# Performance work log

Hardware: AMD Instinct MI355X
Metric: run time of the kernel (lower is better)

The kernel has to match this reference:

```python
import jax, jax.numpy as jnp
import numpy as np

N_NODES = 50000
N_EDGES = 800000
DIM = 128
N_GRAPHS = 512
LEVELS = [2, 2, 2]  # GCN layers per hierarchy level
N_LAYERS = sum(LEVELS)
EPS = 1e-5


def setup_inputs() -> dict:
    key = jax.random.key(0)
    ks = jax.random.split(key, 8)
    x = jax.random.normal(ks[0], (N_NODES, DIM), dtype=jnp.float32)
    edge_index = jax.random.randint(ks[1], (2, N_EDGES), 0, N_NODES, dtype=jnp.int64)
    batch = jnp.sort(jax.random.randint(ks[2], (N_NODES,), 0, N_GRAPHS, dtype=jnp.int64))
    # stacked per-layer GCN params (all layers are DIM->DIM since input_dim==hidden_dim)
    s = 1.0 / np.sqrt(DIM)
    W = jax.random.uniform(ks[3], (N_LAYERS, DIM, DIM), minval=-s, maxval=s, dtype=jnp.float32)
    b = jnp.zeros((N_LAYERS, DIM), dtype=jnp.float32)
    gamma = jnp.ones((N_LAYERS, DIM), dtype=jnp.float32)
    beta = jnp.zeros((N_LAYERS, DIM), dtype=jnp.float32)
    sf = 1.0 / np.sqrt(DIM * len(LEVELS))
    Wf = jax.random.uniform(ks[4], (DIM * len(LEVELS), DIM), minval=-sf, maxval=sf, dtype=jnp.float32)
    bf = jnp.zeros((DIM,), dtype=jnp.float32)
    return {"x": x, "edge_index": edge_index, "batch": batch,
            "W": W, "b": b, "gamma": gamma, "beta": beta, "Wf": Wf, "bf": bf}


def reference(x, edge_index, batch, W, b, gamma, beta, Wf, bf):
    N = x.shape[0]
    # GCNConv: add self-loops, symmetric normalization deg^-1/2 A_hat deg^-1/2
    loop = jnp.arange(N, dtype=edge_index.dtype)
    src = jnp.concatenate([edge_index[0], loop])
    dst = jnp.concatenate([edge_index[1], loop])
    deg = jax.ops.segment_sum(jnp.ones_like(dst, dtype=x.dtype), dst, num_segments=N)
    dinv = jnp.where(deg > 0, jax.lax.rsqrt(deg), 0.0)
    norm = dinv[src] * dinv[dst]  # (E+N,)

    def gcn(h, Wl, bl):
        h = h @ Wl                                   # (N, DIM)
        msg = h[src] * norm[:, None]                 # gather + scale, (E+N, DIM)
        return jax.ops.segment_sum(msg, dst, num_segments=N) + bl

    def batchnorm_relu(h, g, be):
        mu = jnp.mean(h, axis=0)
        var = jnp.mean(jnp.square(h - mu), axis=0)   # biased var (training-mode BN)
        return jax.nn.relu(g * (h - mu) * jax.lax.rsqrt(var + EPS) + be)

    counts = jax.ops.segment_sum(jnp.ones((N,), x.dtype), batch, num_segments=N_GRAPHS)
    counts = jnp.maximum(counts, 1.0)[:, None]

    reps = []
    h = x
    li = 0
    for num_layers in LEVELS:
        for _ in range(num_layers):
            h = batchnorm_relu(gcn(h, W[li], b[li]), gamma[li], beta[li])
            li += 1
        reps.append(jax.ops.segment_sum(h, batch, num_segments=N_GRAPHS) / counts)
    fused = jnp.concatenate(reps, axis=1)            # (G, 3*DIM)
    return jax.nn.relu(fused @ Wf + bf)              # dropout is identity at inference
```

## Files before the change

kernel.cpp:

```cpp
#include <hip/hip_runtime.h>
#include <hip/hip_fp16.h>


#define DIM 128
#define NGRAPH 512
#define EPSV 1e-5f

typedef _Float16 f16x8 __attribute__((ext_vector_type(8)));
typedef float f32x4 __attribute__((ext_vector_type(4)));


__global__ __launch_bounds__(256) void k_count(const int* __restrict__ ei, int* __restrict__ cnt, int E) {
  int e = blockIdx.x * 256 + threadIdx.x;
  if (e < E) atomicAdd(&cnt[ei[E + e]], 1);
}

__global__ __launch_bounds__(512) void k_blocksum(const int* __restrict__ cnt, int* __restrict__ partial, int N) {
  __shared__ int sd[512];
  int idx = blockIdx.x * 512 + threadIdx.x;
  int v = (idx < N) ? cnt[idx] : 0;
  sd[threadIdx.x] = v;
  __syncthreads();
  for (int ofs = 256; ofs > 0; ofs >>= 1) {
    if (threadIdx.x < ofs) sd[threadIdx.x] += sd[threadIdx.x + ofs];
    __syncthreads();
  }
  if (threadIdx.x == 0) partial[blockIdx.x] = sd[0];
}

__global__ __launch_bounds__(128) void k_scanpartials(int* __restrict__ partial, int nb) {
  __shared__ int sp[128];
  int t = threadIdx.x;
  int v = (t < nb) ? partial[t] : 0;
  sp[t] = v;
  __syncthreads();
  for (int ofs = 1; ofs < 128; ofs <<= 1) {
    int a = (t >= ofs) ? sp[t - ofs] : 0;
    __syncthreads();
    sp[t] += a;
    __syncthreads();
  }
  if (t < nb) partial[t] = sp[t] - v;
}

__global__ __launch_bounds__(512) void k_scan_write(const int* __restrict__ cnt, const int* __restrict__ partial,
                                                    int* __restrict__ rowptr, float* __restrict__ dinv, int N) {
  __shared__ int sd[512];
  int tid = threadIdx.x;
  int idx = blockIdx.x * 512 + tid;
  int v = (idx < N) ? cnt[idx] : 0;
  sd[tid] = v;
  __syncthreads();
  for (int ofs = 1; ofs < 512; ofs <<= 1) {
    int a = (tid >= ofs) ? sd[tid - ofs] : 0;
    __syncthreads();
    sd[tid] += a;
    __syncthreads();
  }
  if (idx < N) {
    int excl = partial[blockIdx.x] + sd[tid] - v;
    rowptr[idx] = excl;
    dinv[idx] = rsqrtf((float)(v + 1));
    if (idx == N - 1) rowptr[N] = excl + v;
  }
}

__global__ __launch_bounds__(256) void k_fill(const int* __restrict__ ei, const int* __restrict__ rowptr,
                                              int* __restrict__ cursor, unsigned short* __restrict__ cols, int E) {
  int e = blockIdx.x * 256 + threadIdx.x;
  if (e >= E) return;
  int s = ei[e];
  int d = ei[E + e];
  int pos = rowptr[d] + atomicAdd(&cursor[d], 1);
  cols[pos] = (unsigned short)s;
}

__global__ __launch_bounds__(256) void k_gstart(const int* __restrict__ batch, int* __restrict__ start, int N) {
  int i = blockIdx.x * 256 + threadIdx.x;
  if (i >= N) return;
  int bi = batch[i];
  int prev = (i == 0) ? -1 : batch[i - 1];
  for (int g = prev + 1; g <= bi; ++g) start[g] = i;
  if (i == N - 1) {
    for (int g = bi + 1; g <= NGRAPH; ++g) start[g] = N;
  }
}

__global__ __launch_bounds__(512) void k_invcnt(const int* __restrict__ start, float* __restrict__ invcnt) {
  int g = threadIdx.x;
  if (g < NGRAPH) {
    int c = start[g + 1] - start[g];
    invcnt[g] = 1.0f / (float)max(c, 1);
  }
}

__global__ __launch_bounds__(256) void k_prepw(const float* __restrict__ W, _Float16* __restrict__ W16T) {
  int idx = blockIdx.x * 256 + threadIdx.x;
  if (idx >= 6 * 16384) return;
  int l = idx >> 14, rem = idx & 16383;
  int k = rem >> 7, n = rem & 127;
  W16T[(size_t)l * 16384 + (size_t)n * 128 + k] = (_Float16)W[(size_t)l * 16384 + (size_t)k * 128 + n];
}


#define PITCH 136

__global__ __launch_bounds__(256) void k_gemm(const float* __restrict__ A32,
                                              const unsigned int* __restrict__ A16,
                                              const _Float16* __restrict__ W16T,
                                              const float* __restrict__ statsPrev,
                                              const float* __restrict__ gammaP, const float* __restrict__ betaP,
                                              const float* __restrict__ dinv,
                                              unsigned int* __restrict__ T, int N) {
  __shared__ _Float16 sW[128 * PITCH];
  __shared__ _Float16 sA[64 * PITCH];
  __shared__ float sScSh[256];
  int tid = threadIdx.x;
  size_t pstride = (size_t)(N + 1) * 16;
  if (blockIdx.x == 0 && tid < 64) {
    int p = tid >> 4, sl = tid & 15;
    T[(size_t)p * pstride + (size_t)N * 16 + sl] = 0u;
  }
  if (statsPrev && tid < 128) {
    float invN = 1.f / (float)N;
    float mu = statsPrev[tid] * invN;
    float var = statsPrev[128 + tid] * invN - mu * mu;
    float sc = gammaP[tid] * rsqrtf(var + EPSV);
    sScSh[tid] = sc;
    sScSh[128 + tid] = betaP[tid] - mu * sc;
  }
#pragma unroll
  for (int i = 0; i < 16; ++i) {
    int f = (tid + i * 256) * 4;
    int n = f >> 7, k = f & 127;
    *(uint2*)&sW[n * PITCH + k] = *(const uint2*)&W16T[n * 128 + k];
  }
  __syncthreads();
  int row0 = blockIdx.x * 64;
#pragma unroll
  for (int i = 0; i < 8; ++i) {
    int f = (tid + i * 256) * 4;
    int r = f >> 7, c = f & 127;
    int row = row0 + r;
    uint2 outp = make_uint2(0u, 0u);
    if (row < N) {
      float v0, v1, v2, v3;
      if (statsPrev) {
        uint2 u = *(const uint2*)&A16[(size_t)row * 64 + (c >> 1)];
        float2 lo = __half22float2(*(__half2*)&u.x);
        float2 hi = __half22float2(*(__half2*)&u.y);
        v0 = fmaxf(fmaf(lo.x, sScSh[c], sScSh[128 + c]), 0.f);
        v1 = fmaxf(fmaf(lo.y, sScSh[c + 1], sScSh[128 + c + 1]), 0.f);
        v2 = fmaxf(fmaf(hi.x, sScSh[c + 2], sScSh[128 + c + 2]), 0.f);
        v3 = fmaxf(fmaf(hi.y, sScSh[c + 3], sScSh[128 + c + 3]), 0.f);
      } else {
        float4 v = *(const float4*)&A32[(size_t)row * 128 + c];
        v0 = v.x; v1 = v.y; v2 = v.z; v3 = v.w;
      }
      __half2 h0 = __floats2half2_rn(v0, v1);
      __half2 h1 = __floats2half2_rn(v2, v3);
      outp = make_uint2(*(unsigned int*)&h0, *(unsigned int*)&h1);
    }
    *(uint2*)&sA[r * PITCH + c] = outp;
  }
  __syncthreads();
  int w = tid >> 6;
  int l = tid & 63;
  int m = l & 15, kg = l >> 4;
  int rowbase = 16 * w;
  f16x8 af[4];
#pragma unroll
  for (int ks = 0; ks < 4; ++ks)
    af[ks] = *(const f16x8*)&sA[(rowbase + m) * PITCH + ks * 32 + kg * 8];
  f32x4 acc[8] = {};
#pragma unroll
  for (int t8 = 0; t8 < 8; ++t8) {
#pragma unroll
    for (int ks = 0; ks < 4; ++ks) {
      f16x8 bf = *(const f16x8*)&sW[(t8 * 16 + m) * PITCH + ks * 32 + kg * 8];
      acc[t8] = __builtin_amdgcn_mfma_f32_16x16x32_f16(af[ks], bf, acc[t8], 0, 0, 0);
    }
  }
  float dv[4];
#pragma unroll
  for (int j = 0; j < 4; ++j) {
    int row = row0 + rowbase + kg * 4 + j;
    dv[j] = (row < N) ? dinv[row] : 0.f;
  }
#pragma unroll
  for (int t8 = 0; t8 < 8; ++t8) {
#pragma unroll
    for (int j = 0; j < 4; ++j)
      sA[(rowbase + kg * 4 + j) * PITCH + t8 * 16 + m] = (_Float16)(acc[t8][j] * dv[j]);
  }
  __syncthreads();
#pragma unroll
  for (int i = 0; i < 8; ++i) {
    int idx = tid + i * 256;
    int r = idx >> 5, q = idx & 31;
    int row = row0 + r;
    if (row < N) {
      uint2 val = *(const uint2*)((const char*)sA + r * (PITCH * 2) + q * 8);
      int p = q >> 3, psl = (q & 7) * 2;
      *(uint2*)&T[(size_t)p * pstride + (size_t)row * 16 + psl] = val;
    }
  }
}

__global__ __launch_bounds__(256) void k_agg(const unsigned int* __restrict__ T, const int* __restrict__ rowptr,
                                             const unsigned short* __restrict__ cols, const float* __restrict__ dinv,
                                             const float* __restrict__ bias, unsigned int* __restrict__ hout,
                                             float* __restrict__ stats, int N) {
  int phase = blockIdx.x & 3;
  int chunk = blockIdx.x >> 2;
  int nchunks = gridDim.x >> 2;
  int tid = threadIdx.x;
  int wid = __builtin_amdgcn_readfirstlane(tid >> 6);
  int lane = tid & 63;
  int sub = lane >> 4;
  int slot = lane & 15;
  const unsigned int* __restrict__ Tp = T + (size_t)phase * (N + 1) * 16;
  float bx = bias[phase * 32 + 2 * slot];
  float by = bias[phase * 32 + 2 * slot + 1];
  int gwave = chunk * 4 + wid;
  int nwaves = nchunks * 4;
  float sum0 = 0.f, sum1 = 0.f, sq0 = 0.f, sq1 = 0.f;
  for (int i = gwave; i < N; i += nwaves) {
    float ax = 0.f, ay = 0.f;
    if (sub == 0) {
      unsigned int u0 = Tp[(size_t)i * 16 + slot];
      float2 t0 = __half22float2(*(__half2*)&u0);
      ax = t0.x;
      ay = t0.y;
    }
    int beg = rowptr[i], end = rowptr[i + 1];
    for (int e0 = beg; e0 < end; e0 += 32) {
      int ss[8];
#pragma unroll
      for (int k = 0; k < 8; ++k) {
        int eidx = e0 + 4 * k + sub;
        int cv = (int)cols[eidx];
        ss[k] = (eidx < end) ? cv : N;
      }
      unsigned int uu[8];
#pragma unroll
      for (int k = 0; k < 8; ++k) uu[k] = Tp[(size_t)ss[k] * 16 + slot];
#pragma unroll
      for (int k = 0; k < 8; ++k) {
        float2 t = __half22float2(*(__half2*)&uu[k]);
        ax += t.x;
        ay += t.y;
      }
    }
    ax += __shfl_xor(ax, 16);
    ay += __shfl_xor(ay, 16);
    ax += __shfl_xor(ax, 32);
    ay += __shfl_xor(ay, 32);
    if (sub == 0) {
      float di = dinv[i];
      ax = fmaf(di, ax, bx);
      ay = fmaf(di, ay, by);
      __half2 hp = __floats2half2_rn(ax, ay);
      hout[(size_t)i * 64 + phase * 16 + slot] = *(unsigned int*)&hp;
      sum0 += ax;
      sum1 += ay;
      sq0 = fmaf(ax, ax, sq0);
      sq1 = fmaf(ay, ay, sq1);
    }
  }
  __shared__ float red[4][16][4];
  if (sub == 0) {
    red[wid][slot][0] = sum0;
    red[wid][slot][1] = sum1;
    red[wid][slot][2] = sq0;
    red[wid][slot][3] = sq1;
  }
  __syncthreads();
  if (tid < 16) {
    int sl = tid;
    float a0 = red[0][sl][0] + red[1][sl][0] + red[2][sl][0] + red[3][sl][0];
    float a1 = red[0][sl][1] + red[1][sl][1] + red[2][sl][1] + red[3][sl][1];
    float q0 = red[0][sl][2] + red[1][sl][2] + red[2][sl][2] + red[3][sl][2];
    float q1 = red[0][sl][3] + red[1][sl][3] + red[2][sl][3] + red[3][sl][3];
    int c0 = phase * 32 + 2 * sl;
    atomicAdd(&stats[c0], a0);
    atomicAdd(&stats[c0 + 1], a1);
    atomicAdd(&stats[DIM + c0], q0);
    atomicAdd(&stats[DIM + c0 + 1], q1);
  }
}

__global__ __launch_bounds__(512) void k_pool(const unsigned int* __restrict__ h16, const int* __restrict__ start,
                                              const float* __restrict__ invcnt, const float* __restrict__ statsL,
                                              const float* __restrict__ gammaL, const float* __restrict__ betaL,
                                              float* __restrict__ pooled, int level, int N) {
  int g = blockIdx.x;
  int s = start[g], e = start[g + 1];
  int slot = threadIdx.x & 63;
  int stripe = threadIdx.x >> 6;
  float invN = 1.f / (float)N;
  int c0 = 2 * slot, c1 = c0 + 1;
  float mu0 = statsL[c0] * invN, mu1 = statsL[c1] * invN;
  float var0 = statsL[DIM + c0] * invN - mu0 * mu0;
  float var1 = statsL[DIM + c1] * invN - mu1 * mu1;
  float scx = gammaL[c0] * rsqrtf(var0 + EPSV);
  float scy = gammaL[c1] * rsqrtf(var1 + EPSV);
  float shx = betaL[c0] - mu0 * scx;
  float shy = betaL[c1] - mu1 * scy;
  float ax = 0.f, ay = 0.f;
  for (int r = s + stripe; r < e; r += 8) {
    unsigned int u = h16[(size_t)r * 64 + slot];
    float2 t = __half22float2(*(__half2*)&u);
    ax += fmaxf(fmaf(t.x, scx, shx), 0.f);
    ay += fmaxf(fmaf(t.y, scy, shy), 0.f);
  }
  __shared__ float red[8][64][2];
  red[stripe][slot][0] = ax;
  red[stripe][slot][1] = ay;
  __syncthreads();
  if (threadIdx.x < 64) {
    int sl = threadIdx.x;
    float vx = 0.f, vy = 0.f;
#pragma unroll
    for (int st = 0; st < 8; ++st) {
      vx += red[st][sl][0];
      vy += red[st][sl][1];
    }
    float ic = invcnt[g];
    float* dst = pooled + (size_t)g * (3 * DIM) + level * DIM + 2 * sl;
    dst[0] = vx * ic;
    dst[1] = vy * ic;
  }
}

__global__ __launch_bounds__(512) void k_final(const float* __restrict__ pooled, const float* __restrict__ Wf,
                                               const float* __restrict__ bf, float* __restrict__ out) {
  int t = blockIdx.x * 512 + threadIdx.x;
  if (t >= NGRAPH * DIM) return;
  int j = t & (DIM - 1);
  int i = t >> 7;
  const float* prow = pooled + (size_t)i * (3 * DIM);
  float acc = bf[j];
  for (int k = 0; k < 3 * DIM; ++k) acc = fmaf(prow[k], Wf[(size_t)k * DIM + j], acc);
  out[t] = fmaxf(acc, 0.f);
}


extern "C" void kernel_launch(void* const* d_in, const int* in_sizes, int n_in,
                              void* d_out, int out_size, void* d_ws, size_t ws_size,
                              hipStream_t stream) {
  const float* x = (const float*)d_in[0];
  const int* ei = (const int*)d_in[1];
  const int* batch = (const int*)d_in[2];
  const float* W = (const float*)d_in[3];
  const float* b = (const float*)d_in[4];
  const float* gamma = (const float*)d_in[5];
  const float* beta = (const float*)d_in[6];
  const float* Wf = (const float*)d_in[7];
  const float* bf = (const float*)d_in[8];
  float* out = (float*)d_out;

  const int N = in_sizes[0] / DIM;
  const int E = in_sizes[1] / 2;

  char* base = (char*)d_ws;
  size_t off = 0;
  auto alloc = [&](size_t bytes) -> char* {
    char* p = base + off;
    off += (bytes + 255) & ~(size_t)255;
    return p;
  };
  unsigned int* h16 = (unsigned int*)alloc((size_t)N * DIM * 2);
  unsigned int* T   = (unsigned int*)alloc((size_t)(N + 1) * DIM * 2);
  _Float16* W16T    = (_Float16*)alloc((size_t)6 * 16384 * 2);
  int* cnt          = (int*)alloc((size_t)N * 4);
  int* cursor       = (int*)alloc((size_t)N * 4);
  int* rowptr       = (int*)alloc((size_t)(N + 1) * 4);
  int* partial      = (int*)alloc(256 * 4);
  float* dinv       = (float*)alloc((size_t)N * 4);
  unsigned short* cols = (unsigned short*)alloc((size_t)(E + 32) * 2);
  float* statsAll   = (float*)alloc(6 * 256 * 4);
  int* start        = (int*)alloc((NGRAPH + 1) * 4);
  float* invcnt     = (float*)alloc(NGRAPH * 4);
  float* pooled     = (float*)alloc((size_t)NGRAPH * 3 * DIM * 4);
  (void)ws_size;

  (void)hipMemsetAsync(cnt, 0, (size_t)N * 4, stream);
  (void)hipMemsetAsync(cursor, 0, (size_t)N * 4, stream);
  (void)hipMemsetAsync(statsAll, 0, 6 * 256 * 4, stream);

  int nbScan = (N + 511) / 512;
  k_count<<<(E + 255) / 256, 256, 0, stream>>>(ei, cnt, E);
  k_blocksum<<<nbScan, 512, 0, stream>>>(cnt, partial, N);
  k_scanpartials<<<1, 128, 0, stream>>>(partial, nbScan);
  k_scan_write<<<nbScan, 512, 0, stream>>>(cnt, partial, rowptr, dinv, N);
  k_fill<<<(E + 255) / 256, 256, 0, stream>>>(ei, rowptr, cursor, cols, E);
  k_gstart<<<(N + 255) / 256, 256, 0, stream>>>(batch, start, N);
  k_invcnt<<<1, 512, 0, stream>>>(start, invcnt);
  k_prepw<<<(6 * 16384 + 255) / 256, 256, 0, stream>>>(W, W16T);

  int gemmGrid = (N + 63) / 64;
  for (int l = 0; l < 6; ++l) {
    const float* statsPrev = (l == 0) ? nullptr : statsAll + (l - 1) * 256;
    const float* gP = (l == 0) ? gamma : gamma + (size_t)(l - 1) * DIM;
    const float* bP = (l == 0) ? beta : beta + (size_t)(l - 1) * DIM;
    k_gemm<<<gemmGrid, 256, 0, stream>>>((l == 0) ? x : nullptr, (l == 0) ? nullptr : h16,
                                         W16T + (size_t)l * 16384, statsPrev, gP, bP, dinv, T, N);
    k_agg<<<2048, 256, 0, stream>>>(T, rowptr, cols, dinv, b + (size_t)l * DIM, h16,
                                    statsAll + (size_t)l * 256, N);
    if (l & 1)
      k_pool<<<NGRAPH, 512, 0, stream>>>(h16, start, invcnt, statsAll + (size_t)l * 256,
                                         gamma + (size_t)l * DIM, beta + (size_t)l * DIM,
                                         pooled, l >> 1, N);
  }
  k_final<<<(NGRAPH * DIM + 511) / 512, 512, 0, stream>>>(pooled, Wf, bf, out);
}
```

Before: 693.6 us.

## Pad CSR rows to multiples of sixteen with self-loop and sentinel fill

Each CSR row is padded to a multiple of 16 slots, with the self-loop stored as the first entry and the unused slots filled with a sentinel that points at the zero row of T. This lets the aggregation loop read 4 column indices per lane with one 64-bit load and drop the per-edge bounds checks and the separate self-loop load. The cost is extra padded gathers (about 8 wasted slots per row on average at degree ~17), a larger cols buffer, and two more setup kernels.

```diff
diff --git a/kernel.cpp b/kernel.cpp
--- a/kernel.cpp
+++ b/kernel.cpp
@@ -15,10 +15,12 @@
   if (e < E) atomicAdd(&cnt[ei[E + e]], 1);
 }
 
+__device__ inline int padslots(int deg) { return (deg + 16) & ~15; }
+
 __global__ __launch_bounds__(512) void k_blocksum(const int* __restrict__ cnt, int* __restrict__ partial, int N) {
   __shared__ int sd[512];
   int idx = blockIdx.x * 512 + threadIdx.x;
-  int v = (idx < N) ? cnt[idx] : 0;
+  int v = (idx < N) ? padslots(cnt[idx]) : 0;
   sd[threadIdx.x] = v;
   __syncthreads();
   for (int ofs = 256; ofs > 0; ofs >>= 1) {
@@ -48,7 +50,8 @@
   __shared__ int sd[512];
   int tid = threadIdx.x;
   int idx = blockIdx.x * 512 + tid;
-  int v = (idx < N) ? cnt[idx] : 0;
+  int raw = (idx < N) ? cnt[idx] : 0;
+  int v = (idx < N) ? padslots(raw) : 0;
   sd[tid] = v;
   __syncthreads();
   for (int ofs = 1; ofs < 512; ofs <<= 1) {
@@ -60,9 +63,22 @@
   if (idx < N) {
     int excl = partial[blockIdx.x] + sd[tid] - v;
     rowptr[idx] = excl;
-    dinv[idx] = rsqrtf((float)(v + 1));
+    dinv[idx] = rsqrtf((float)(raw + 1));
     if (idx == N - 1) rowptr[N] = excl + v;
   }
+}
+
+__global__ __launch_bounds__(256) void k_colsinit(unsigned int* __restrict__ cols32, int n32, unsigned int val) {
+  int i = blockIdx.x * 256 + threadIdx.x;
+  if (i < n32) cols32[i] = val;
+}
+
+__global__ __launch_bounds__(256) void k_selfinit(const int* __restrict__ rowptr, int* __restrict__ cursor,
+                                                  unsigned short* __restrict__ cols, int N) {
+  int i = blockIdx.x * 256 + threadIdx.x;
+  if (i >= N) return;
+  cursor[i] = 1;
+  cols[rowptr[i]] = (unsigned short)i;
 }
 
 __global__ __launch_bounds__(256) void k_fill(const int* __restrict__ ei, const int* __restrict__ rowptr,
@@ -227,30 +243,25 @@
   float sum0 = 0.f, sum1 = 0.f, sq0 = 0.f, sq1 = 0.f;
   for (int i = gwave; i < N; i += nwaves) {
     float ax = 0.f, ay = 0.f;
-    if (sub == 0) {
-      unsigned int u0 = Tp[(size_t)i * 16 + slot];
+    int beg = rowptr[i];
+    int nb = (rowptr[i + 1] - beg) >> 4;
+    const unsigned short* cp = cols + beg + sub * 4;
+    for (int b = 0; b < nb; ++b, cp += 16) {
+      uint2 cw = *(const uint2*)cp;
+      int s0 = cw.x & 0xFFFF, s1 = cw.x >> 16;
+      int s2 = cw.y & 0xFFFF, s3 = cw.y >> 16;
+      unsigned int u0 = Tp[(size_t)s0 * 16 + slot];
+      unsigned int u1 = Tp[(size_t)s1 * 16 + slot];
+      unsigned int u2 = Tp[(size_t)s2 * 16 + slot];
+      unsigned int u3 = Tp[(size_t)s3 * 16 + slot];
       float2 t0 = __half22float2(*(__half2*)&u0);
-      ax = t0.x;
-      ay = t0.y;
-    }
-    int beg = rowptr[i], end = rowptr[i + 1];
-    for (int e0 = beg; e0 < end; e0 += 32) {
-      int ss[8];
-#pragma unroll
-      for (int k = 0; k < 8; ++k) {
-        int eidx = e0 + 4 * k + sub;
-        int cv = (int)cols[eidx];
-        ss[k] = (eidx < end) ? cv : N;
-      }
-      unsigned int uu[8];
-#pragma unroll
-      for (int k = 0; k < 8; ++k) uu[k] = Tp[(size_t)ss[k] * 16 + slot];
-#pragma unroll
-      for (int k = 0; k < 8; ++k) {
-        float2 t = __half22float2(*(__half2*)&uu[k]);
-        ax += t.x;
-        ay += t.y;
-      }
+      float2 t1 = __half22float2(*(__half2*)&u1);
+      float2 t2 = __half22float2(*(__half2*)&u2);
+      float2 t3 = __half22float2(*(__half2*)&u3);
+      ax += t0.x + t1.x;
+      ay += t0.y + t1.y;
+      ax += t2.x + t3.x;
+      ay += t2.y + t3.y;
     }
     ax += __shfl_xor(ax, 16);
     ay += __shfl_xor(ay, 16);
@@ -370,6 +381,7 @@
     off += (bytes + 255) & ~(size_t)255;
     return p;
   };
+  const size_t colsCap = (size_t)E + 16 * (size_t)N + 64;
   unsigned int* h16 = (unsigned int*)alloc((size_t)N * DIM * 2);
   unsigned int* T   = (unsigned int*)alloc((size_t)(N + 1) * DIM * 2);
   _Float16* W16T    = (_Float16*)alloc((size_t)6 * 16384 * 2);
@@ -378,7 +390,7 @@
   int* rowptr       = (int*)alloc((size_t)(N + 1) * 4);
   int* partial      = (int*)alloc(256 * 4);
   float* dinv       = (float*)alloc((size_t)N * 4);
-  unsigned short* cols = (unsigned short*)alloc((size_t)(E + 32) * 2);
+  unsigned short* cols = (unsigned short*)alloc(colsCap * 2);
   float* statsAll   = (float*)alloc(6 * 256 * 4);
   int* start        = (int*)alloc((NGRAPH + 1) * 4);
   float* invcnt     = (float*)alloc(NGRAPH * 4);
@@ -386,7 +398,6 @@
   (void)ws_size;
 
   (void)hipMemsetAsync(cnt, 0, (size_t)N * 4, stream);
-  (void)hipMemsetAsync(cursor, 0, (size_t)N * 4, stream);
   (void)hipMemsetAsync(statsAll, 0, 6 * 256 * 4, stream);
 
   int nbScan = (N + 511) / 512;
@@ -394,6 +405,10 @@
   k_blocksum<<<nbScan, 512, 0, stream>>>(cnt, partial, N);
   k_scanpartials<<<1, 128, 0, stream>>>(partial, nbScan);
   k_scan_write<<<nbScan, 512, 0, stream>>>(cnt, partial, rowptr, dinv, N);
+  int n32 = (int)(colsCap / 2);
+  unsigned int sentinel = ((unsigned int)N << 16) | (unsigned int)N;
+  k_colsinit<<<(n32 + 255) / 256, 256, 0, stream>>>((unsigned int*)cols, n32, sentinel);
+  k_selfinit<<<(N + 255) / 256, 256, 0, stream>>>(rowptr, cursor, cols, N);
   k_fill<<<(E + 255) / 256, 256, 0, stream>>>(ei, rowptr, cursor, cols, E);
   k_gstart<<<(N + 255) / 256, 256, 0, stream>>>(batch, start, N);
   k_invcnt<<<1, 512, 0, stream>>>(start, invcnt);
```

Measured after the change: 670.1 us. 1.04x faster.
